# Kernel tuning notes

Hardware: AMD Instinct MI355X
Metric: run time of the kernel (lower is better)

The kernel has to match this reference:

```python
import jax, jax.numpy as jnp
import numpy as np

B, S, E, H = 1024, 64, 1024, 16  # batch, seq (n_agent+1), n_embd, num_heads
D = E // H  # head_dim = 64


def setup_inputs() -> dict:
    k = jax.random.key(0)
    ks = jax.random.split(k, 7)
    w = lambda i: jax.random.normal(ks[i], (E, E), jnp.float32) * 0.02
    return {
        "query": jax.random.normal(ks[0], (B, S, E), jnp.float32),
        "key": jax.random.normal(ks[1], (B, S, E), jnp.float32),
        "value": jax.random.normal(ks[2], (B, S, E), jnp.float32),
        "Wq": w(3), "bq": jnp.zeros((E,), jnp.float32),
        "Wk": w(4), "bk": jnp.zeros((E,), jnp.float32),
        "Wv": w(5), "bv": jnp.zeros((E,), jnp.float32),
        "Wo": w(6), "bo": jnp.zeros((E,), jnp.float32),
    }


def reference(query, key, value, Wq, bq, Wk, bk, Wv, bv, Wo, bo):
    Bq, Q, _ = query.shape
    K = key.shape[1]
    # projections -> [B, H, L, D]
    q = (query @ Wq + bq).reshape(Bq, Q, H, D).transpose(0, 2, 1, 3)
    k = (key @ Wk + bk).reshape(Bq, K, H, D).transpose(0, 2, 1, 3)
    v = (value @ Wv + bv).reshape(Bq, K, H, D).transpose(0, 2, 1, 3)
    # non-standard: ReLU on Q and K before scores
    q = jnp.maximum(q, 0.0)
    k = jnp.maximum(k, 0.0)
    scale = 1.0 / jnp.sqrt(jnp.float32(D))
    scores = jnp.einsum('bhqd,bhkd->bhqk', q, k) * scale  # [B,H,Q,K]
    # causal mask (tril of the (n_agent+1)^2 mask, sliced to q_len,kv_len)
    mask = jnp.tril(jnp.ones((Q, K), jnp.float32))[None, None]
    scores = jnp.where(mask == 0, jnp.finfo(jnp.float32).min, scores)
    attn = jax.nn.softmax(scores, axis=-1)
    out = jnp.einsum('bhqk,bhkd->bhqd', attn, v)
    out = out.transpose(0, 2, 1, 3).reshape(Bq, Q, E)
    return out @ Wo + bo
```

## Files before the change

kernel.cpp:

```cpp
#include <hip/hip_runtime.h>

typedef __attribute__((ext_vector_type(4))) float f32x4;
typedef __attribute__((ext_vector_type(8))) short short8;
typedef __attribute__((ext_vector_type(2))) unsigned int uint2v;

#define MFMA_BF16(a,b,c) __builtin_amdgcn_mfma_f32_16x16x32_bf16(a,b,c,0,0,0)

__device__ __forceinline__ unsigned short bf16_of(float f) {
  union { float f; unsigned int u; } v; v.f = f;
  unsigned int r = v.u + 0x7fffu + ((v.u >> 16) & 1u);
  return (unsigned short)(r >> 16);
}

__device__ __forceinline__ unsigned int cvt_pk_bf16(float lo, float hi) {
  unsigned int r;
  asm("v_cvt_pk_bf16_f32 %0, %1, %2" : "=v"(r) : "v"(lo), "v"(hi));
  return r;
}

__device__ __forceinline__ int swz(int r) { return (r + (r >> 2)) & 3; }

__device__ __forceinline__ void gload_lds16(const void* g, void* l) {
  __builtin_amdgcn_global_load_lds(
      (const __attribute__((address_space(1))) unsigned int*)g,
      (__attribute__((address_space(3))) unsigned int*)l, 16, 0, 0);
}

__global__ __launch_bounds__(256)
void wcast_kernel(const float* __restrict__ W0, const float* __restrict__ W1,
                  const float* __restrict__ W2, const float* __restrict__ W3,
                  unsigned short* __restrict__ wt) {
  __shared__ float tile[64][65];
  const float* W = (blockIdx.z == 0) ? W0 : (blockIdx.z == 1) ? W1
                 : (blockIdx.z == 2) ? W2 : W3;
  unsigned short* Wt = wt + (size_t)blockIdx.z * (1024u * 1024u);
  int k0 = blockIdx.x * 64, n0 = blockIdx.y * 64;
  int t = threadIdx.x, r = t >> 6, c = t & 63;
#pragma unroll
  for (int i = 0; i < 16; ++i)
    tile[r + i * 4][c] = W[(size_t)(k0 + r + i * 4) * 1024 + n0 + c];
  __syncthreads();
#pragma unroll
  for (int i = 0; i < 16; ++i)
    Wt[(size_t)(n0 + r + i * 4) * 1024 + k0 + c] = bf16_of(tile[c][r + i * 4]);
}

template <int MODE>
__global__ __launch_bounds__(256, 4)
void gemm_kernel(const void* __restrict__ A_, const unsigned short* __restrict__ Bt,
                 const float* __restrict__ bias, void* __restrict__ C_) {
  constexpr bool AF32 = (MODE != 2);
  __shared__ unsigned short ldsA[128 * 32];
  __shared__ unsigned short ldsB[128 * 32];

  int bid = blockIdx.x;
  int mt = (bid & 7) * 64 + (bid >> 6);
  int nt = (bid >> 3) & 7;
  int m0 = mt * 128, n0 = nt * 128;

  int tid = threadIdx.x;
  int w = tid >> 6, l = tid & 63;
  int wm = w >> 1, wn = w & 1;
  int li = l & 15, grp = l >> 4;

  f32x4 acc[4][4] = {};

  const float* Af = (const float*)A_;
  const unsigned short* Ab = (const unsigned short*)A_;

  int ar = tid >> 3;
  int ac4 = tid & 7;
  int rA = l >> 2;
  int pseg = l & 3;

  f32x4 areg[4];
  if constexpr (AF32) {
#pragma unroll
    for (int i = 0; i < 4; ++i)
      areg[i] = *(const f32x4*)(Af + (size_t)(m0 + ar + 32 * i) * 1024 + ac4 * 4);
  }

  for (int kt = 0; kt < 32; ++kt) {
    int k0 = kt * 32;
    if constexpr (AF32) {
#pragma unroll
      for (int i = 0; i < 4; ++i) {
        int row = ar + 32 * i;
        uint2v pk;
        pk.x = cvt_pk_bf16(areg[i][0], areg[i][1]);
        pk.y = cvt_pk_bf16(areg[i][2], areg[i][3]);
        int seg = ac4 >> 1, sub = ac4 & 1;
        int off = row * 64 + ((seg ^ swz(row)) << 4) + sub * 8;
        *(uint2v*)((char*)ldsA + off) = pk;
      }
    } else {
#pragma unroll
      for (int i = 0; i < 2; ++i) {
        int c = w * 2 + i;
        int row = c * 16 + rA;
        int s = pseg ^ swz(row);
        gload_lds16(Ab + (size_t)(m0 + row) * 1024 + k0 + s * 8,
                    (char*)ldsA + c * 1024);
      }
    }
#pragma unroll
    for (int i = 0; i < 2; ++i) {
      int c = w * 2 + i;
      int row = c * 16 + rA;
      int s = pseg ^ swz(row);
      gload_lds16(Bt + (size_t)(n0 + row) * 1024 + k0 + s * 8,
                  (char*)ldsB + c * 1024);
    }
    if constexpr (AF32) {
      if (kt < 31) {
#pragma unroll
        for (int i = 0; i < 4; ++i)
          areg[i] = *(const f32x4*)(Af + (size_t)(m0 + ar + 32 * i) * 1024 + (k0 + 32) + ac4 * 4);
      }
    }
    __syncthreads();
    short8 af[4], bf[4];
#pragma unroll
    for (int mi = 0; mi < 4; ++mi) {
      int row = wm * 64 + mi * 16 + li;
      af[mi] = *(const short8*)((const char*)ldsA + row * 64 + ((grp ^ swz(row)) << 4));
    }
#pragma unroll
    for (int ni = 0; ni < 4; ++ni) {
      int row = wn * 64 + ni * 16 + li;
      bf[ni] = *(const short8*)((const char*)ldsB + row * 64 + ((grp ^ swz(row)) << 4));
    }
#pragma unroll
    for (int mi = 0; mi < 4; ++mi)
#pragma unroll
      for (int ni = 0; ni < 4; ++ni)
        acc[mi][ni] = MFMA_BF16(af[mi], bf[ni], acc[mi][ni]);
    __syncthreads();
  }

  int mrow0 = m0 + wm * 64;
  int ncol0 = n0 + wn * 64;
  float bvv[4];
#pragma unroll
  for (int ni = 0; ni < 4; ++ni) bvv[ni] = bias[ncol0 + ni * 16 + li];

  if constexpr (MODE == 2) {
    float* C = (float*)C_;
#pragma unroll
    for (int mi = 0; mi < 4; ++mi)
#pragma unroll
      for (int ni = 0; ni < 4; ++ni)
#pragma unroll
        for (int j = 0; j < 4; ++j)
          C[(size_t)(mrow0 + mi * 16 + grp * 4 + j) * 1024 + ncol0 + ni * 16 + li] =
              acc[mi][ni][j] + bvv[ni];
  } else if constexpr (MODE == 0) {
    unsigned short* C = (unsigned short*)C_;
    int b = mrow0 >> 6, h = ncol0 >> 6;
    unsigned short* base = C + (size_t)b * 65536 + (size_t)h * 4096;
#pragma unroll
    for (int mi = 0; mi < 4; ++mi)
#pragma unroll
      for (int ni = 0; ni < 4; ++ni)
#pragma unroll
        for (int j = 0; j < 4; ++j) {
          float v = acc[mi][ni][j] + bvv[ni];
          v = fmaxf(v, 0.0f);
          base[(mi * 16 + grp * 4 + j) * 64 + ni * 16 + li] = bf16_of(v);
        }
  } else {
    unsigned short* C = (unsigned short*)C_;
    int b = mrow0 >> 6, h = ncol0 >> 6;
    unsigned short* base = C + (size_t)b * 65536 + (size_t)h * 4096;
#pragma unroll
    for (int mi = 0; mi < 4; ++mi)
#pragma unroll
      for (int ni = 0; ni < 4; ++ni) {
        uint2v pk;
        pk.x = cvt_pk_bf16(acc[mi][ni][0] + bvv[ni], acc[mi][ni][1] + bvv[ni]);
        pk.y = cvt_pk_bf16(acc[mi][ni][2] + bvv[ni], acc[mi][ni][3] + bvv[ni]);
        *(uint2v*)(base + (ni * 16 + li) * 64 + mi * 16 + grp * 4) = pk;
      }
  }
}

__global__ __launch_bounds__(64)
void attn_kernel(const unsigned short* __restrict__ qw,
                 const unsigned short* __restrict__ kw,
                 const unsigned short* __restrict__ vw,
                 unsigned short* __restrict__ aw) {
  __shared__ unsigned short p_lds[64 * 72];
  int bh = blockIdx.x;
  int b = bh >> 4, h = bh & 15;
  int l = threadIdx.x;
  int li = l & 15, grp = l >> 4;
  const unsigned short* qb = qw + (size_t)bh * 4096;
  const unsigned short* kb = kw + (size_t)bh * 4096;
  const unsigned short* vb = vw + (size_t)bh * 4096;

  short8 aq[4][2], bk_[4][2];
#pragma unroll
  for (int mi = 0; mi < 4; ++mi)
#pragma unroll
    for (int ks = 0; ks < 2; ++ks) {
      aq[mi][ks]  = *(const short8*)(qb + (mi * 16 + li) * 64 + ks * 32 + grp * 8);
      bk_[mi][ks] = *(const short8*)(kb + (mi * 16 + li) * 64 + ks * 32 + grp * 8);
    }

  f32x4 sf[4][4];
#pragma unroll
  for (int mi = 0; mi < 4; ++mi)
#pragma unroll
    for (int ni = 0; ni < 4; ++ni) {
      f32x4 t = {};
      t = MFMA_BF16(aq[mi][0], bk_[ni][0], t);
      t = MFMA_BF16(aq[mi][1], bk_[ni][1], t);
      sf[mi][ni] = t;
    }

#pragma unroll
  for (int mi = 0; mi < 4; ++mi) {
#pragma unroll
    for (int j = 0; j < 4; ++j) {
      int row = mi * 16 + grp * 4 + j;
      float mx = -1e30f;
#pragma unroll
      for (int ni = 0; ni < 4; ++ni) {
        int col = ni * 16 + li;
        float v = sf[mi][ni][j] * 0.125f;
        v = (col <= row) ? v : -1e30f;
        sf[mi][ni][j] = v;
        mx = fmaxf(mx, v);
      }
#pragma unroll
      for (int sh = 1; sh < 16; sh <<= 1) mx = fmaxf(mx, __shfl_xor(mx, sh, 64));
      float sum = 0.0f;
#pragma unroll
      for (int ni = 0; ni < 4; ++ni) {
        float e = __expf(sf[mi][ni][j] - mx);
        sf[mi][ni][j] = e;
        sum += e;
      }
#pragma unroll
      for (int sh = 1; sh < 16; sh <<= 1) sum += __shfl_xor(sum, sh, 64);
      float rr = 1.0f / sum;
#pragma unroll
      for (int ni = 0; ni < 4; ++ni) sf[mi][ni][j] *= rr;
    }
  }

#pragma unroll
  for (int mi = 0; mi < 4; ++mi)
#pragma unroll
    for (int ni = 0; ni < 4; ++ni)
#pragma unroll
      for (int j = 0; j < 4; ++j)
        p_lds[(mi * 16 + grp * 4 + j) * 72 + ni * 16 + li] = bf16_of(sf[mi][ni][j]);
  __syncthreads();

  short8 pa[4][2], bv_[4][2];
#pragma unroll
  for (int mi = 0; mi < 4; ++mi)
#pragma unroll
    for (int ks = 0; ks < 2; ++ks)
      pa[mi][ks] = *(const short8*)(p_lds + (mi * 16 + li) * 72 + ks * 32 + grp * 8);
#pragma unroll
  for (int ni = 0; ni < 4; ++ni)
#pragma unroll
    for (int ks = 0; ks < 2; ++ks)
      bv_[ni][ks] = *(const short8*)(vb + (ni * 16 + li) * 64 + ks * 32 + grp * 8);

  f32x4 of[4][4];
#pragma unroll
  for (int mi = 0; mi < 4; ++mi)
#pragma unroll
    for (int ni = 0; ni < 4; ++ni) {
      f32x4 t = {};
      t = MFMA_BF16(pa[mi][0], bv_[ni][0], t);
      t = MFMA_BF16(pa[mi][1], bv_[ni][1], t);
      of[mi][ni] = t;
    }

  unsigned short* ab = aw + (size_t)b * 65536 + (size_t)h * 64;
#pragma unroll
  for (int mi = 0; mi < 4; ++mi)
#pragma unroll
    for (int ni = 0; ni < 4; ++ni)
#pragma unroll
      for (int j = 0; j < 4; ++j)
        ab[(size_t)(mi * 16 + grp * 4 + j) * 1024 + ni * 16 + li] = bf16_of(of[mi][ni][j]);
}

extern "C" void kernel_launch(void* const* d_in, const int* in_sizes, int n_in,
                              void* d_out, int out_size, void* d_ws, size_t ws_size,
                              hipStream_t stream) {
  (void)in_sizes; (void)n_in; (void)out_size; (void)ws_size;
  const float* query = (const float*)d_in[0];
  const float* key   = (const float*)d_in[1];
  const float* value = (const float*)d_in[2];
  const float* Wq = (const float*)d_in[3];
  const float* bq = (const float*)d_in[4];
  const float* Wk = (const float*)d_in[5];
  const float* bk = (const float*)d_in[6];
  const float* Wv = (const float*)d_in[7];
  const float* bv = (const float*)d_in[8];
  const float* Wo = (const float*)d_in[9];
  const float* bo = (const float*)d_in[10];
  float* out = (float*)d_out;

  unsigned short* wt = (unsigned short*)d_ws;
  const size_t NE = (size_t)67108864;
  unsigned short* qw = wt + (size_t)4 * 1024 * 1024;
  unsigned short* kw = qw + NE;
  unsigned short* vw = kw + NE;
  unsigned short* aw = vw + NE;

  wcast_kernel<<<dim3(16, 16, 4), 256, 0, stream>>>(Wq, Wk, Wv, Wo, wt);
  gemm_kernel<0><<<dim3(4096), 256, 0, stream>>>(query, wt + (size_t)0 * 1048576, bq, qw);
  gemm_kernel<0><<<dim3(4096), 256, 0, stream>>>(key,   wt + (size_t)1 * 1048576, bk, kw);
  gemm_kernel<1><<<dim3(4096), 256, 0, stream>>>(value, wt + (size_t)2 * 1048576, bv, vw);
  attn_kernel<<<dim3(16384), 64, 0, stream>>>(qw, kw, vw, aw);
  gemm_kernel<2><<<dim3(4096), 256, 0, stream>>>(aw, wt + (size_t)3 * 1048576, bo, out);
}
```

Measured before the change: 1.003 ms.

## Enlarge GEMM tiles to 128x256 with K-step 64 and 512 threads

The projection GEMMs now use 128x256 output tiles, 8 waves per block, and a 64-wide K step with an 8-way XOR LDS swizzle. Reuse of each staged A tile goes up, and the number of k-iterations and barriers is halved. In exchange, LDS use per block and register pressure rise, and fewer blocks are launched, which may reduce occupancy.

```diff
diff --git a/kernel.cpp b/kernel.cpp
--- a/kernel.cpp
+++ b/kernel.cpp
@@ -3,6 +3,7 @@
 typedef __attribute__((ext_vector_type(4))) float f32x4;
 typedef __attribute__((ext_vector_type(8))) short short8;
 typedef __attribute__((ext_vector_type(2))) unsigned int uint2v;
+typedef __attribute__((ext_vector_type(4))) unsigned int uint4v;
 
 #define MFMA_BF16(a,b,c) __builtin_amdgcn_mfma_f32_16x16x32_bf16(a,b,c,0,0,0)
 
@@ -17,8 +18,6 @@
   asm("v_cvt_pk_bf16_f32 %0, %1, %2" : "=v"(r) : "v"(lo), "v"(hi));
   return r;
 }
-
-__device__ __forceinline__ int swz(int r) { return (r + (r >> 2)) & 3; }
 
 __device__ __forceinline__ void gload_lds16(const void* g, void* l) {
   __builtin_amdgcn_global_load_lds(
@@ -46,21 +45,21 @@
 }
 
 template <int MODE>
-__global__ __launch_bounds__(256, 4)
+__global__ __launch_bounds__(512, 4)
 void gemm_kernel(const void* __restrict__ A_, const unsigned short* __restrict__ Bt,
                  const float* __restrict__ bias, void* __restrict__ C_) {
   constexpr bool AF32 = (MODE != 2);
-  __shared__ unsigned short ldsA[128 * 32];
-  __shared__ unsigned short ldsB[128 * 32];
+  __shared__ unsigned short ldsA[128 * 64];
+  __shared__ unsigned short ldsB[256 * 64];
 
   int bid = blockIdx.x;
-  int mt = (bid & 7) * 64 + (bid >> 6);
-  int nt = (bid >> 3) & 7;
-  int m0 = mt * 128, n0 = nt * 128;
+  int mt = (bid & 7) * 64 + (bid >> 5);
+  int nt = (bid >> 3) & 3;
+  int m0 = mt * 128, n0 = nt * 256;
 
   int tid = threadIdx.x;
   int w = tid >> 6, l = tid & 63;
-  int wm = w >> 1, wn = w & 1;
+  int wm = w >> 2, wn = w & 3;
   int li = l & 15, grp = l >> 4;
 
   f32x4 acc[4][4] = {};
@@ -68,73 +67,75 @@
   const float* Af = (const float*)A_;
   const unsigned short* Ab = (const unsigned short*)A_;
 
-  int ar = tid >> 3;
-  int ac4 = tid & 7;
-  int rA = l >> 2;
-  int pseg = l & 3;
+  int grow = l >> 3;
+  int gseg = (l & 7) ^ grow;
+
+  int rA = tid >> 2, q = tid & 3;
 
   f32x4 areg[4];
   if constexpr (AF32) {
 #pragma unroll
-    for (int i = 0; i < 4; ++i)
-      areg[i] = *(const f32x4*)(Af + (size_t)(m0 + ar + 32 * i) * 1024 + ac4 * 4);
+    for (int j = 0; j < 4; ++j)
+      areg[j] = *(const f32x4*)(Af + (size_t)(m0 + rA) * 1024 + q * 16 + j * 4);
   }
 
-  for (int kt = 0; kt < 32; ++kt) {
-    int k0 = kt * 32;
+  for (int kt = 0; kt < 16; ++kt) {
+    int k0 = kt * 64;
     if constexpr (AF32) {
-#pragma unroll
-      for (int i = 0; i < 4; ++i) {
-        int row = ar + 32 * i;
-        uint2v pk;
-        pk.x = cvt_pk_bf16(areg[i][0], areg[i][1]);
-        pk.y = cvt_pk_bf16(areg[i][2], areg[i][3]);
-        int seg = ac4 >> 1, sub = ac4 & 1;
-        int off = row * 64 + ((seg ^ swz(row)) << 4) + sub * 8;
-        *(uint2v*)((char*)ldsA + off) = pk;
-      }
+      uint4v w0, w1;
+      w0[0] = cvt_pk_bf16(areg[0][0], areg[0][1]);
+      w0[1] = cvt_pk_bf16(areg[0][2], areg[0][3]);
+      w0[2] = cvt_pk_bf16(areg[1][0], areg[1][1]);
+      w0[3] = cvt_pk_bf16(areg[1][2], areg[1][3]);
+      w1[0] = cvt_pk_bf16(areg[2][0], areg[2][1]);
+      w1[1] = cvt_pk_bf16(areg[2][2], areg[2][3]);
+      w1[2] = cvt_pk_bf16(areg[3][0], areg[3][1]);
+      w1[3] = cvt_pk_bf16(areg[3][2], areg[3][3]);
+      *(uint4v*)((char*)ldsA + rA * 128 + (((2 * q)     ^ (rA & 7)) << 4)) = w0;
+      *(uint4v*)((char*)ldsA + rA * 128 + (((2 * q + 1) ^ (rA & 7)) << 4)) = w1;
     } else {
 #pragma unroll
       for (int i = 0; i < 2; ++i) {
         int c = w * 2 + i;
-        int row = c * 16 + rA;
-        int s = pseg ^ swz(row);
-        gload_lds16(Ab + (size_t)(m0 + row) * 1024 + k0 + s * 8,
+        gload_lds16(Ab + (size_t)(m0 + 8 * c + grow) * 1024 + k0 + gseg * 8,
                     (char*)ldsA + c * 1024);
       }
     }
 #pragma unroll
-    for (int i = 0; i < 2; ++i) {
-      int c = w * 2 + i;
-      int row = c * 16 + rA;
-      int s = pseg ^ swz(row);
-      gload_lds16(Bt + (size_t)(n0 + row) * 1024 + k0 + s * 8,
+    for (int i = 0; i < 4; ++i) {
+      int c = w * 4 + i;
+      gload_lds16(Bt + (size_t)(n0 + 8 * c + grow) * 1024 + k0 + gseg * 8,
                   (char*)ldsB + c * 1024);
     }
     if constexpr (AF32) {
-      if (kt < 31) {
-#pragma unroll
-        for (int i = 0; i < 4; ++i)
-          areg[i] = *(const f32x4*)(Af + (size_t)(m0 + ar + 32 * i) * 1024 + (k0 + 32) + ac4 * 4);
+      if (kt < 15) {
+#pragma unroll
+        for (int j = 0; j < 4; ++j)
+          areg[j] = *(const f32x4*)(Af + (size_t)(m0 + rA) * 1024 + (k0 + 64) + q * 16 + j * 4);
       }
     }
     __syncthreads();
-    short8 af[4], bf[4];
-#pragma unroll
-    for (int mi = 0; mi < 4; ++mi) {
-      int row = wm * 64 + mi * 16 + li;
-      af[mi] = *(const short8*)((const char*)ldsA + row * 64 + ((grp ^ swz(row)) << 4));
-    }
-#pragma unroll
-    for (int ni = 0; ni < 4; ++ni) {
-      int row = wn * 64 + ni * 16 + li;
-      bf[ni] = *(const short8*)((const char*)ldsB + row * 64 + ((grp ^ swz(row)) << 4));
-    }
-#pragma unroll
-    for (int mi = 0; mi < 4; ++mi)
-#pragma unroll
-      for (int ni = 0; ni < 4; ++ni)
-        acc[mi][ni] = MFMA_BF16(af[mi], bf[ni], acc[mi][ni]);
+#pragma unroll
+    for (int ks = 0; ks < 2; ++ks) {
+      short8 af[4], bf[4];
+#pragma unroll
+      for (int mi = 0; mi < 4; ++mi) {
+        int row = wm * 64 + mi * 16 + li;
+        af[mi] = *(const short8*)((const char*)ldsA + row * 128 +
+                                  (((ks * 4 + grp) ^ (row & 7)) << 4));
+      }
+#pragma unroll
+      for (int ni = 0; ni < 4; ++ni) {
+        int row = wn * 64 + ni * 16 + li;
+        bf[ni] = *(const short8*)((const char*)ldsB + row * 128 +
+                                  (((ks * 4 + grp) ^ (row & 7)) << 4));
+      }
+#pragma unroll
+      for (int mi = 0; mi < 4; ++mi)
+#pragma unroll
+        for (int ni = 0; ni < 4; ++ni)
+          acc[mi][ni] = MFMA_BF16(af[mi], bf[ni], acc[mi][ni]);
+    }
     __syncthreads();
   }
 
@@ -316,9 +317,9 @@
   unsigned short* aw = vw + NE;
 
   wcast_kernel<<<dim3(16, 16, 4), 256, 0, stream>>>(Wq, Wk, Wv, Wo, wt);
-  gemm_kernel<0><<<dim3(4096), 256, 0, stream>>>(query, wt + (size_t)0 * 1048576, bq, qw);
-  gemm_kernel<0><<<dim3(4096), 256, 0, stream>>>(key,   wt + (size_t)1 * 1048576, bk, kw);
-  gemm_kernel<1><<<dim3(4096), 256, 0, stream>>>(value, wt + (size_t)2 * 1048576, bv, vw);
+  gemm_kernel<0><<<dim3(2048), 512, 0, stream>>>(query, wt + (size_t)0 * 1048576, bq, qw);
+  gemm_kernel<0><<<dim3(2048), 512, 0, stream>>>(key,   wt + (size_t)1 * 1048576, bk, kw);
+  gemm_kernel<1><<<dim3(2048), 512, 0, stream>>>(value, wt + (size_t)2 * 1048576, bv, vw);
   attn_kernel<<<dim3(16384), 64, 0, stream>>>(qw, kw, vw, aw);
-  gemm_kernel<2><<<dim3(4096), 256, 0, stream>>>(aw, wt + (size_t)3 * 1048576, bo, out);
-}
+  gemm_kernel<2><<<dim3(2048), 512, 0, stream>>>(aw, wt + (size_t)3 * 1048576, bo, out);
+}
```

Measured after the change: 923.3 us. 8.0% less time.

## Double-buffer GEMM LDS tiles and drop the second per-iteration barrier

Applied to the files above, without the earlier changes.

Splits the A and B LDS tiles into two buffers so the next K-slice is staged while the current one feeds MFMA, leaving one __syncthreads per iteration instead of two. The fp32 A path now has each thread load a half row of 16 floats and write it with 128-bit LDS stores. The swizzle changes from (r + r>>2)&3 to (r>>1)&3 for the new store pattern. This doubles LDS use per block (32 KB), which may reduce occupancy below the launch-bounds target of 4, and the new swizzle may cause different bank conflicts.

```diff
diff --git a/kernel.cpp b/kernel.cpp
--- a/kernel.cpp
+++ b/kernel.cpp
@@ -3,6 +3,7 @@
 typedef __attribute__((ext_vector_type(4))) float f32x4;
 typedef __attribute__((ext_vector_type(8))) short short8;
 typedef __attribute__((ext_vector_type(2))) unsigned int uint2v;
+typedef __attribute__((ext_vector_type(4))) unsigned int uint4v;
 
 #define MFMA_BF16(a,b,c) __builtin_amdgcn_mfma_f32_16x16x32_bf16(a,b,c,0,0,0)
 
@@ -17,8 +18,6 @@
   asm("v_cvt_pk_bf16_f32 %0, %1, %2" : "=v"(r) : "v"(lo), "v"(hi));
   return r;
 }
-
-__device__ __forceinline__ int swz(int r) { return (r + (r >> 2)) & 3; }
 
 __device__ __forceinline__ void gload_lds16(const void* g, void* l) {
   __builtin_amdgcn_global_load_lds(
@@ -50,8 +49,8 @@
 void gemm_kernel(const void* __restrict__ A_, const unsigned short* __restrict__ Bt,
                  const float* __restrict__ bias, void* __restrict__ C_) {
   constexpr bool AF32 = (MODE != 2);
-  __shared__ unsigned short ldsA[128 * 32];
-  __shared__ unsigned short ldsB[128 * 32];
+  __shared__ unsigned short ldsA[2][4096];
+  __shared__ unsigned short ldsB[2][4096];
 
   int bid = blockIdx.x;
   int mt = (bid & 7) * 64 + (bid >> 6);
@@ -68,74 +67,87 @@
   const float* Af = (const float*)A_;
   const unsigned short* Ab = (const unsigned short*)A_;
 
-  int ar = tid >> 3;
-  int ac4 = tid & 7;
-  int rA = l >> 2;
-  int pseg = l & 3;
-
-  f32x4 areg[4];
-  if constexpr (AF32) {
-#pragma unroll
-    for (int i = 0; i < 4; ++i)
-      areg[i] = *(const f32x4*)(Af + (size_t)(m0 + ar + 32 * i) * 1024 + ac4 * 4);
-  }
-
-  for (int kt = 0; kt < 32; ++kt) {
-    int k0 = kt * 32;
-    if constexpr (AF32) {
-#pragma unroll
-      for (int i = 0; i < 4; ++i) {
-        int row = ar + 32 * i;
-        uint2v pk;
-        pk.x = cvt_pk_bf16(areg[i][0], areg[i][1]);
-        pk.y = cvt_pk_bf16(areg[i][2], areg[i][3]);
-        int seg = ac4 >> 1, sub = ac4 & 1;
-        int off = row * 64 + ((seg ^ swz(row)) << 4) + sub * 8;
-        *(uint2v*)((char*)ldsA + off) = pk;
-      }
-    } else {
-#pragma unroll
-      for (int i = 0; i < 2; ++i) {
-        int c = w * 2 + i;
-        int row = c * 16 + rA;
-        int s = pseg ^ swz(row);
-        gload_lds16(Ab + (size_t)(m0 + row) * 1024 + k0 + s * 8,
-                    (char*)ldsA + c * 1024);
-      }
-    }
+  int grow = l >> 2;
+  int gslot = l & 3;
+
+  int rA = tid >> 1, q = tid & 1;
+  int sA = (rA >> 1) & 3;
+
+  auto stageB = [&](int buf, int kt) {
 #pragma unroll
     for (int i = 0; i < 2; ++i) {
       int c = w * 2 + i;
-      int row = c * 16 + rA;
-      int s = pseg ^ swz(row);
-      gload_lds16(Bt + (size_t)(n0 + row) * 1024 + k0 + s * 8,
-                  (char*)ldsB + c * 1024);
-    }
-    if constexpr (AF32) {
-      if (kt < 31) {
-#pragma unroll
-        for (int i = 0; i < 4; ++i)
-          areg[i] = *(const f32x4*)(Af + (size_t)(m0 + ar + 32 * i) * 1024 + (k0 + 32) + ac4 * 4);
-      }
-    }
+      int row = c * 16 + grow;
+      int seg = gslot ^ ((row >> 1) & 3);
+      gload_lds16(Bt + (size_t)(n0 + row) * 1024 + kt * 32 + seg * 8,
+                  (char*)&ldsB[buf][0] + c * 1024);
+    }
+  };
+  auto stageAg = [&](int buf, int kt) {
+#pragma unroll
+    for (int i = 0; i < 2; ++i) {
+      int c = w * 2 + i;
+      int row = c * 16 + grow;
+      int seg = gslot ^ ((row >> 1) & 3);
+      gload_lds16(Ab + (size_t)(m0 + row) * 1024 + kt * 32 + seg * 8,
+                  (char*)&ldsA[buf][0] + c * 1024);
+    }
+  };
+
+  f32x4 areg[4];
+  auto loadA = [&](int kt) {
+#pragma unroll
+    for (int j = 0; j < 4; ++j)
+      areg[j] = *(const f32x4*)(Af + (size_t)(m0 + rA) * 1024 + kt * 32 + q * 16 + j * 4);
+  };
+  auto writeA = [&](int buf) {
+    uint4v w0, w1;
+    w0[0] = cvt_pk_bf16(areg[0][0], areg[0][1]);
+    w0[1] = cvt_pk_bf16(areg[0][2], areg[0][3]);
+    w0[2] = cvt_pk_bf16(areg[1][0], areg[1][1]);
+    w0[3] = cvt_pk_bf16(areg[1][2], areg[1][3]);
+    w1[0] = cvt_pk_bf16(areg[2][0], areg[2][1]);
+    w1[1] = cvt_pk_bf16(areg[2][2], areg[2][3]);
+    w1[2] = cvt_pk_bf16(areg[3][0], areg[3][1]);
+    w1[3] = cvt_pk_bf16(areg[3][2], areg[3][3]);
+    *(uint4v*)((char*)&ldsA[buf][0] + rA * 64 + (((2 * q)     ^ sA) << 4)) = w0;
+    *(uint4v*)((char*)&ldsA[buf][0] + rA * 64 + (((2 * q + 1) ^ sA) << 4)) = w1;
+  };
+
+  stageB(0, 0);
+  if constexpr (AF32) { loadA(0); writeA(0); }
+  else                { stageAg(0, 0); }
+
+  for (int kt = 0; kt < 32; ++kt) {
+    int cur = kt & 1;
     __syncthreads();
+    if (kt < 31) {
+      stageB(cur ^ 1, kt + 1);
+      if constexpr (AF32) loadA(kt + 1);
+      else                stageAg(cur ^ 1, kt + 1);
+      __builtin_amdgcn_sched_barrier(0);
+    }
     short8 af[4], bf[4];
 #pragma unroll
     for (int mi = 0; mi < 4; ++mi) {
       int row = wm * 64 + mi * 16 + li;
-      af[mi] = *(const short8*)((const char*)ldsA + row * 64 + ((grp ^ swz(row)) << 4));
+      af[mi] = *(const short8*)((const char*)&ldsA[cur][0] + row * 64 +
+                                ((grp ^ ((row >> 1) & 3)) << 4));
     }
 #pragma unroll
     for (int ni = 0; ni < 4; ++ni) {
       int row = wn * 64 + ni * 16 + li;
-      bf[ni] = *(const short8*)((const char*)ldsB + row * 64 + ((grp ^ swz(row)) << 4));
+      bf[ni] = *(const short8*)((const char*)&ldsB[cur][0] + row * 64 +
+                                ((grp ^ ((row >> 1) & 3)) << 4));
     }
 #pragma unroll
     for (int mi = 0; mi < 4; ++mi)
 #pragma unroll
       for (int ni = 0; ni < 4; ++ni)
         acc[mi][ni] = MFMA_BF16(af[mi], bf[ni], acc[mi][ni]);
-    __syncthreads();
+    if constexpr (AF32) {
+      if (kt < 31) writeA(cur ^ 1);
+    }
   }
 
   int mrow0 = m0 + wm * 64;
```

Result: slower. 1.074 ms (+7.1%).
